# Kernel optimization log

Hardware: AMD Instinct MI355X
Metric: run time of the kernel (lower is better)

## Reference

```python
import jax, jax.numpy as jnp
import numpy as np

DIM = 192
K = 3
RED = 4
B, H, W = 4, 256, 256
EPS = 1e-5  # BatchNorm eps

def _make_mask():
    # PixelCNN mask type 'A': zero the center pixel and everything after it
    m = np.ones((DIM, 1, K, K), np.float32)
    m[:, :, K // 2, K // 2:] = 0.0  # center row: center col onward
    m[:, :, K // 2 + 1:] = 0.0      # all rows below center
    return jnp.asarray(m)

MASK = _make_mask()  # [DIM, 1, K, K]

def setup_inputs() -> dict:
    key = jax.random.key(0)
    ks = jax.random.split(key, 4)
    r = DIM // RED
    return {
        "x": jax.random.normal(ks[0], (B, DIM, H, W), jnp.float32),
        "w1": jax.random.normal(ks[1], (r, DIM), jnp.float32) * 0.05,      # conv1 1x1, no bias
        "gamma": jnp.ones((r,), jnp.float32),                               # BN weight
        "beta": jnp.zeros((r,), jnp.float32),                               # BN bias
        "running_mean": jnp.zeros((r,), jnp.float32),
        "running_var": jnp.ones((r,), jnp.float32),
        "w2": jax.random.normal(ks[2], (DIM * K * K, r), jnp.float32) * 0.05,  # conv2 1x1
        "b2": jnp.zeros((DIM * K * K,), jnp.float32),
        "bias": jnp.zeros((DIM,), jnp.float32),                             # depthwise conv bias
    }

def reference(x, w1, gamma, beta, running_mean, running_var, w2, b2, bias):
    b, c, h, w = x.shape  # c == DIM
    # --- dynamic weight generation: pool -> 1x1 conv -> BN(eval) -> ReLU -> 1x1 conv ---
    pooled = x.mean(axis=(2, 3))                                   # [b, dim]
    t = pooled @ w1.T                                              # [b, dim//red]
    t = gamma * (t - running_mean) * jax.lax.rsqrt(running_var + EPS) + beta
    t = jax.nn.relu(t)
    wt = t @ w2.T + b2                                             # [b, dim*K*K]
    wt = wt.reshape(b * DIM, 1, K, K) * jnp.tile(MASK, (b, 1, 1, 1))
    # --- per-sample masked depthwise conv via batch-folding (groups = b*dim) ---
    out = jax.lax.conv_general_dilated(
        x.reshape(1, b * c, h, w), wt,
        window_strides=(1, 1), padding=((1, 1), (1, 1)),
        feature_group_count=b * DIM,
        dimension_numbers=("NCHW", "OIHW", "NCHW"))                # [1, b*dim, h, w]
    out = out + jnp.tile(bias, (b,))[None, :, None, None]
    return out.reshape(b, c, h, w)
```

## Files before the change

### kernel.cpp

```cpp
#include <hip/hip_runtime.h>

#define DIMC 192
#define HID  48
#define HW   65536
#define WIDTH 256
#define NPLANE 768

typedef float nfloat4 __attribute__((ext_vector_type(4)));

__global__ __launch_bounds__(1024) void k_pool(const float* __restrict__ x,
                                               float* __restrict__ pooled) {
    const int plane = blockIdx.x;
    const float4* p = (const float4*)(x + (size_t)plane * HW);
    const int t = threadIdx.x;
    float s = 0.f;
#pragma unroll
    for (int k = 0; k < 16; ++k) {
        float4 v = p[k * 1024 + t];
        s += (v.x + v.y) + (v.z + v.w);
    }
#pragma unroll
    for (int off = 32; off > 0; off >>= 1) s += __shfl_down(s, off, 64);
    __shared__ float wsum[16];
    const int wave = t >> 6, lane = t & 63;
    if (lane == 0) wsum[wave] = s;
    __syncthreads();
    if (t == 0) {
        float tot = 0.f;
#pragma unroll
        for (int i = 0; i < 16; ++i) tot += wsum[i];
        pooled[plane] = tot * (1.0f / 65536.0f);
    }
}

__global__ __launch_bounds__(256) void k_conv(
    const float* __restrict__ x,
    const float* __restrict__ pooled,
    const float* __restrict__ w1,
    const float* __restrict__ gamma,
    const float* __restrict__ beta,
    const float* __restrict__ rmean,
    const float* __restrict__ rvar,
    const float* __restrict__ w2,
    const float* __restrict__ b2,
    const float* __restrict__ bias,
    float* __restrict__ out)
{
    const int plane = blockIdx.x >> 3;
    const int b = plane / DIMC;
    const int c = plane - b * DIMC;
    const int tid = threadIdx.x;

    __shared__ float T[HID];
    __shared__ float W4[4];
    {
        const int g = tid >> 2, l = tid & 3;
        if (g < HID) {
            const float* pr = pooled + b * DIMC;
            const float* wr = w1 + g * DIMC;
            float acc = 0.f;
#pragma unroll 8
            for (int d = l; d < DIMC; d += 4) acc += pr[d] * wr[d];
            acc += __shfl_xor(acc, 1, 64);
            acc += __shfl_xor(acc, 2, 64);
            if (l == 0) {
                const float inv = rsqrtf(rvar[g] + 1e-5f);
                float v = gamma[g] * (acc - rmean[g]) * inv + beta[g];
                T[g] = v > 0.f ? v : 0.f;
            }
        }
        __syncthreads();
        if (tid < 4) {
            const int o = c * 9 + tid;
            const float* wr = w2 + o * HID;
            float acc = b2[o];
#pragma unroll
            for (int j = 0; j < HID; ++j) acc += T[j] * wr[j];
            W4[tid] = acc;
        }
        __syncthreads();
    }
    const float4 wt = make_float4(W4[0], W4[1], W4[2], W4[3]);
    const float bs = bias[c];

    const int wave = tid >> 6;
    const int lane = tid & 63;
    const int y0 = ((blockIdx.x & 7) << 5) + (wave << 3);
    const float4* xp = (const float4*)(x + (size_t)plane * HW);
    nfloat4* op = (nfloat4*)(out + (size_t)plane * HW);

    float4 a;
    if (y0 == 0) a = make_float4(0.f, 0.f, 0.f, 0.f);
    else         a = xp[(y0 - 1) * 64 + lane];

#pragma unroll
    for (int r = 0; r < 8; ++r) {
        const int y = y0 + r;
        float4 bb = xp[y * 64 + lane];
        float leftA  = __shfl_up(a.w, 1, 64);   if (lane == 0)  leftA  = 0.f;
        float rightA = __shfl_down(a.x, 1, 64); if (lane == 63) rightA = 0.f;
        float leftB  = __shfl_up(bb.w, 1, 64);  if (lane == 0)  leftB  = 0.f;
        nfloat4 o;
        o.x = wt.x * leftA + wt.y * a.x + wt.z * a.y    + wt.w * leftB + bs;
        o.y = wt.x * a.x   + wt.y * a.y + wt.z * a.z    + wt.w * bb.x  + bs;
        o.z = wt.x * a.y   + wt.y * a.z + wt.z * a.w    + wt.w * bb.y  + bs;
        o.w = wt.x * a.z   + wt.y * a.w + wt.z * rightA + wt.w * bb.z  + bs;
        __builtin_nontemporal_store(o, &op[y * 64 + lane]);
        a = bb;
    }
}

extern "C" void kernel_launch(void* const* d_in, const int* in_sizes, int n_in,
                              void* d_out, int out_size, void* d_ws, size_t ws_size,
                              hipStream_t stream) {
    const float* x     = (const float*)d_in[0];
    const float* w1    = (const float*)d_in[1];
    const float* gamma = (const float*)d_in[2];
    const float* beta  = (const float*)d_in[3];
    const float* rmean = (const float*)d_in[4];
    const float* rvar  = (const float*)d_in[5];
    const float* w2    = (const float*)d_in[6];
    const float* b2    = (const float*)d_in[7];
    const float* bias  = (const float*)d_in[8];
    float* out = (float*)d_out;

    float* pooled = (float*)d_ws;

    k_pool<<<NPLANE, 1024, 0, stream>>>(x, pooled);
    k_conv<<<NPLANE * 8, 256, 0, stream>>>(x, pooled, w1, gamma, beta,
                                           rmean, rvar, w2, b2, bias, out);
}
```

Baseline: 382.4 us.

## Split pool and conv per batch sample to reuse input from cache

```diff
diff --git a/kernel.cpp b/kernel.cpp
--- a/kernel.cpp
+++ b/kernel.cpp
@@ -8,34 +8,31 @@
 
 typedef float nfloat4 __attribute__((ext_vector_type(4)));
 
-__global__ __launch_bounds__(1024) void k_pool(const float* __restrict__ x,
-                                               float* __restrict__ pooled) {
-    const int plane = blockIdx.x;
-    const float4* p = (const float4*)(x + (size_t)plane * HW);
+
+__global__ __launch_bounds__(256) void k_pool_s(const float* __restrict__ xs,
+                                                float* __restrict__ pp) {
+    const int plane = blockIdx.x >> 2;
+    const int strip = blockIdx.x & 3;
+    const float4* p = (const float4*)(xs + (size_t)plane * HW + strip * 64 * WIDTH);
     const int t = threadIdx.x;
     float s = 0.f;
 #pragma unroll
     for (int k = 0; k < 16; ++k) {
-        float4 v = p[k * 1024 + t];
+        float4 v = p[k * 256 + t];
         s += (v.x + v.y) + (v.z + v.w);
     }
 #pragma unroll
     for (int off = 32; off > 0; off >>= 1) s += __shfl_down(s, off, 64);
-    __shared__ float wsum[16];
+    __shared__ float wsum[4];
     const int wave = t >> 6, lane = t & 63;
     if (lane == 0) wsum[wave] = s;
     __syncthreads();
-    if (t == 0) {
-        float tot = 0.f;
-#pragma unroll
-        for (int i = 0; i < 16; ++i) tot += wsum[i];
-        pooled[plane] = tot * (1.0f / 65536.0f);
-    }
+    if (t == 0) pp[blockIdx.x] = (wsum[0] + wsum[1]) + (wsum[2] + wsum[3]);
 }
 
-__global__ __launch_bounds__(256) void k_conv(
-    const float* __restrict__ x,
-    const float* __restrict__ pooled,
+__global__ __launch_bounds__(256) void k_conv_s(
+    const float* __restrict__ xs,
+    const float* __restrict__ pp,
     const float* __restrict__ w1,
     const float* __restrict__ gamma,
     const float* __restrict__ beta,
@@ -44,23 +41,26 @@
     const float* __restrict__ w2,
     const float* __restrict__ b2,
     const float* __restrict__ bias,
-    float* __restrict__ out)
+    float* __restrict__ outs)
 {
-    const int plane = blockIdx.x >> 3;
-    const int b = plane / DIMC;
-    const int c = plane - b * DIMC;
+    const int c = blockIdx.x >> 3;
     const int tid = threadIdx.x;
 
+    __shared__ float P[DIMC];
     __shared__ float T[HID];
     __shared__ float W4[4];
+    if (tid < DIMC) {
+        float4 v = ((const float4*)pp)[tid];
+        P[tid] = ((v.x + v.y) + (v.z + v.w)) * (1.0f / 65536.0f);
+    }
+    __syncthreads();
     {
         const int g = tid >> 2, l = tid & 3;
         if (g < HID) {
-            const float* pr = pooled + b * DIMC;
             const float* wr = w1 + g * DIMC;
             float acc = 0.f;
 #pragma unroll 8
-            for (int d = l; d < DIMC; d += 4) acc += pr[d] * wr[d];
+            for (int d = l; d < DIMC; d += 4) acc += P[d] * wr[d];
             acc += __shfl_xor(acc, 1, 64);
             acc += __shfl_xor(acc, 2, 64);
             if (l == 0) {
@@ -86,8 +86,8 @@
     const int wave = tid >> 6;
     const int lane = tid & 63;
     const int y0 = ((blockIdx.x & 7) << 5) + (wave << 3);
-    const float4* xp = (const float4*)(x + (size_t)plane * HW);
-    nfloat4* op = (nfloat4*)(out + (size_t)plane * HW);
+    const float4* xp = (const float4*)(xs + (size_t)c * HW);
+    nfloat4* op = (nfloat4*)(outs + (size_t)c * HW);
 
     float4 a;
     if (y0 == 0) a = make_float4(0.f, 0.f, 0.f, 0.f);
@@ -124,9 +124,13 @@
     const float* bias  = (const float*)d_in[8];
     float* out = (float*)d_out;
 
-    float* pooled = (float*)d_ws;
+    float* pp = (float*)d_ws;
 
-    k_pool<<<NPLANE, 1024, 0, stream>>>(x, pooled);
-    k_conv<<<NPLANE * 8, 256, 0, stream>>>(x, pooled, w1, gamma, beta,
-                                           rmean, rvar, w2, b2, bias, out);
+    for (int b = 0; b < 4; ++b) {
+        const float* xs = x   + (size_t)b * DIMC * HW;
+        float* outs     = out + (size_t)b * DIMC * HW;
+        k_pool_s<<<768, 256, 0, stream>>>(xs, pp + b * 768);
+        k_conv_s<<<1536, 256, 0, stream>>>(xs, pp + b * 768, w1, gamma, beta,
+                                           rmean, rvar, w2, b2, bias, outs);
+    }
 }
```

After: 410.9 us. 1.07x slower.
